# Kernel optimization log

Measured on AMD Instinct MI355X. Metric: run time of the kernel, lower is better.

Reference implementation:

```python
import jax, jax.numpy as jnp
import numpy as np

B, NPG, NFEAT, NHID, NCLASS = 32, 256, 128, 64, 6
N = B * NPG
E_PER = NPG * 16
C = 1.0
SQC = 1.0  # sqrt(c)
MIN_NORM = 1e-15
PROJ_EPS = 4e-3
LAMB = 1.0


def _norm(x):
    return jnp.clip(jnp.linalg.norm(x, axis=-1, keepdims=True), MIN_NORM)


def artanh(x):
    x = jnp.clip(x, -1.0 + 1e-7, 1.0 - 1e-7)
    return 0.5 * (jnp.log1p(x) - jnp.log1p(-x))


def proj(x):
    # clip points to stay inside the Poincare ball
    n = _norm(x)
    maxn = (1.0 - PROJ_EPS) / SQC
    return jnp.where(n > maxn, x / n * maxn, x)


def expmap0(u):
    un = _norm(u)
    return jnp.tanh(SQC * un) * u / (SQC * un)


def logmap0(p):
    pn = _norm(p)
    return artanh(SQC * pn) * p / (SQC * pn)


def mobius_matvec(W, x):
    xn = _norm(x)
    mx = x @ W.T
    mxn = _norm(mx)
    return jnp.tanh(mxn / xn * artanh(SQC * xn)) * mx / (mxn * SQC)


def mobius_add(x, y):
    x2 = jnp.sum(x * x, -1, keepdims=True)
    y2 = jnp.sum(y * y, -1, keepdims=True)
    xy = jnp.sum(x * y, -1, keepdims=True)
    num = (1.0 + 2.0 * C * xy + C * y2) * x + (1.0 - C * x2) * y
    den = 1.0 + 2.0 * C * xy + C * C * x2 * y2
    return num / jnp.clip(den, MIN_NORM)


def hgc_layer(xh, adj, W, b):
    # HypLinear (mobius matvec + hyperbolic bias)
    h = proj(mobius_matvec(W, xh))
    hb = proj(expmap0(b.reshape(1, -1)))
    h = proj(mobius_add(h, hb))
    # HypAgg: aggregate in tangent space at origin
    h = proj(expmap0(adj @ logmap0(h)))
    # HypAct: relu in tangent space
    return proj(expmap0(jax.nn.relu(logmap0(h))))


def hgpsl_pool(x, adj, att, nb, npg):
    deg = adj.sum(-1)
    dis = jnp.where(deg > 0, deg ** -0.5, 0.0)
    prop = dis[:, None] * (adj @ (dis[:, None] * x))
    score = jnp.abs(x - prop).sum(-1)  # [N]
    k = npg // 2
    vals, idx = jax.lax.top_k(score.reshape(nb, npg), k)  # per-graph top-k
    gidx = (idx + (jnp.arange(nb) * npg)[:, None]).reshape(-1)  # global ids
    xn = x[gidx] * jnp.tanh(vals).reshape(-1, 1)
    adj_ind = adj[gidx][:, gidx]
    # structure learning: single-head additive attention, masked per graph
    d = xn.shape[-1]
    e = jax.nn.leaky_relu((xn @ att[:d])[:, None] + (xn @ att[d:])[None, :], 0.2)
    gid = jnp.repeat(jnp.arange(nb), k)
    mask = gid[:, None] == gid[None, :]
    new_adj = jnp.where(mask, jax.nn.relu(e) + LAMB * adj_ind, 0.0)
    return xn, new_adj


def readout(x, nb, k):
    xr = x.reshape(nb, k, -1)
    return jnp.concatenate([xr.max(axis=1), xr.mean(axis=1)], axis=-1)


def to_hyp(t):
    return proj(expmap0(t))  # proj_tan0 is identity on the Poincare ball


def forward(x, edge_index, W1, b1, W2, b2, W3, b3, att1, att2,
            lw1, lb1, lw2, lb2, lw3, lb3):
    row, col = edge_index[0], edge_index[1]
    w = (x[row].sum(-1) + x[col].sum(-1)) * 0.5
    adj1 = jnp.zeros((N, N), x.dtype).at[row, col].set(w)

    t = logmap0(hgc_layer(to_hyp(x), adj1, W1, b1))
    t, adj2 = hgpsl_pool(t, adj1, att1, B, NPG)
    k1 = NPG // 2
    x1 = readout(t, B, k1)

    t = logmap0(hgc_layer(to_hyp(t), adj2, W2, b2))
    t, adj3 = hgpsl_pool(t, adj2, att2, B, k1)
    k2 = k1 // 2
    x2 = readout(t, B, k2)

    t = logmap0(hgc_layer(to_hyp(t), adj3, W3, b3))
    x3 = readout(t, B, k2)

    r = jax.nn.relu(x1) + jax.nn.relu(x2) + jax.nn.relu(x3)
    r = jax.nn.relu(r @ lw1.T + lb1)
    r = jax.nn.relu(r @ lw2.T + lb2)
    return jax.nn.log_softmax(r @ lw3.T + lb3, axis=-1)


def setup_inputs() -> dict:
    key = jax.random.key(0)
    ks = jax.random.split(key, 16)
    s = 0.1
    x = jax.random.normal(ks[0], (N, NFEAT), jnp.float32)
    off = jnp.repeat(jnp.arange(B, dtype=jnp.int32) * NPG, E_PER)
    row = jax.random.randint(ks[1], (B * E_PER,), 0, NPG, jnp.int32) + off
    col = jax.random.randint(ks[2], (B * E_PER,), 0, NPG, jnp.int32) + off
    edge_index = jnp.stack([row, col])
    return {
        "x": x,
        "edge_index": edge_index,
        "W1": jax.random.normal(ks[3], (NHID, NFEAT), jnp.float32) * s,
        "b1": jax.random.normal(ks[4], (NHID,), jnp.float32) * s,
        "W2": jax.random.normal(ks[5], (NHID, NHID), jnp.float32) * s,
        "b2": jax.random.normal(ks[6], (NHID,), jnp.float32) * s,
        "W3": jax.random.normal(ks[7], (NHID, NHID), jnp.float32) * s,
        "b3": jax.random.normal(ks[8], (NHID,), jnp.float32) * s,
        "att1": jax.random.normal(ks[9], (2 * NHID,), jnp.float32) * s,
        "att2": jax.random.normal(ks[10], (2 * NHID,), jnp.float32) * s,
        "lw1": jax.random.normal(ks[11], (NHID, 2 * NHID), jnp.float32) * s,
        "lb1": jnp.zeros((NHID,), jnp.float32),
        "lw2": jax.random.normal(ks[12], (NHID // 2, NHID), jnp.float32) * s,
        "lb2": jnp.zeros((NHID // 2,), jnp.float32),
        "lw3": jax.random.normal(ks[13], (NCLASS, NHID // 2), jnp.float32) * s,
        "lb3": jnp.zeros((NCLASS,), jnp.float32),
    }


def reference(x, edge_index, W1, b1, W2, b2, W3, b3, att1, att2,
              lw1, lb1, lw2, lb2, lw3, lb3):
    return forward(x, edge_index, W1, b1, W2, b2, W3, b3, att1, att2,
                   lw1, lb1, lw2, lb2, lw3, lb3)
```

## Files before the change

### kernel.cpp

```cpp
#include <hip/hip_runtime.h>
#include <math.h>

#define MAXN 0.996f

__device__ __forceinline__ float wredsum(float v) {
#pragma unroll
  for (int o = 32; o > 0; o >>= 1) v += __shfl_xor(v, o);
  return v;
}

__device__ __forceinline__ float artanh_f(float x) {
  x = fminf(fmaxf(x, -1.0f + 1e-7f), 1.0f - 1e-7f);
  return 0.5f * (log1pf(x) - log1pf(-x));
}

__device__ __forceinline__ float cload(const float* p) {
  return __hip_atomic_load(p, __ATOMIC_RELAXED, __HIP_MEMORY_SCOPE_AGENT);
}
__device__ __forceinline__ int cloadi(const int* p) {
  return __hip_atomic_load(p, __ATOMIC_RELAXED, __HIP_MEMORY_SCOPE_AGENT);
}
__device__ __forceinline__ void cstore(float* p, float v) {
  __hip_atomic_store(p, v, __ATOMIC_RELAXED, __HIP_MEMORY_SCOPE_AGENT);
}
__device__ __forceinline__ void cstorei(int* p, int v) {
  __hip_atomic_store(p, v, __ATOMIC_RELAXED, __HIP_MEMORY_SCOPE_AGENT);
}
__device__ __forceinline__ void cstore64(float* p, float lo, float hi) {
  unsigned long long u =
      ((unsigned long long)__float_as_uint(hi) << 32) | __float_as_uint(lo);
  __hip_atomic_store((unsigned long long*)p, u, __ATOMIC_RELAXED,
                     __HIP_MEMORY_SCOPE_AGENT);
}
__device__ __forceinline__ void pairStore(float* base, int j, float v) {
  float o = __shfl_xor(v, 1);
  if ((j & 1) == 0) cstore64(base + j, v, o);
}
template <int N>
__device__ __forceinline__ void stage64(float* dst, const float* src, int tid) {
  const unsigned long long* s = (const unsigned long long*)src;
  unsigned long long* d = (unsigned long long*)dst;
  unsigned long long v[N];
#pragma unroll
  for (int k = 0; k < N; ++k)
    v[k] = __hip_atomic_load(s + tid + k * 1024, __ATOMIC_RELAXED,
                             __HIP_MEMORY_SCOPE_AGENT);
#pragma unroll
  for (int k = 0; k < N; ++k) d[tid + k * 1024] = v[k];
}

__device__ __forceinline__ float chainB(float acc) {
  float n0 = sqrtf(wredsum(acc * acc));
  float u0 = fmaxf(n0, 1e-15f);
  float e1 = tanhf(u0) / u0;
  float c1 = fmaxf(e1 * n0, 1e-15f);
  float v = acc * e1;
  if (c1 > MAXN) { v *= MAXN / c1; c1 = MAXN; }
  v *= artanh_f(c1) / c1;
  v = fmaxf(v, 0.f);
  float n2 = sqrtf(wredsum(v * v));
  float u2 = fmaxf(n2, 1e-15f);
  float e2 = tanhf(u2) / u2;
  float c2 = fmaxf(e2 * n2, 1e-15f);
  v *= e2;
  if (c2 > MAXN) { v *= MAXN / c2; c2 = MAXN; }
  v *= artanh_f(c2) / c2;
  return v;
}

__device__ __forceinline__ void hbCalc(int j, const float* __restrict__ b,
                                       float& hbj, float& y2) {
  float bj = b[j];
  float nb = sqrtf(wredsum(bj * bj));
  float ub = fmaxf(nb, 1e-15f);
  float eb = tanhf(ub) / ub;
  float cb = fmaxf(eb * nb, 1e-15f);
  hbj = bj * eb * ((cb > MAXN) ? MAXN / cb : 1.0f);
  y2 = wredsum(hbj * hbj);
}

template <int IND>
__device__ __forceinline__ void doArow(int j, const float* xs, const float* wT,
                                       float hbj, float y2,
                                       float* __restrict__ uout) {
  float a2 = xs[j] * xs[j];
  if (IND == 128) { float x1v = xs[64 + j]; a2 += x1v * x1v; }
  float nx = sqrtf(wredsum(a2));
  float un = fmaxf(nx, 1e-15f);
  float s1 = tanhf(un) / un;
  float nv = s1 * nx;
  float nn = fmaxf(nv, 1e-15f);
  float s2 = (nn > MAXN) ? MAXN / nn : 1.0f;
  float alpha = s1 * s2;
  float xn = fmaxf(fminf(nn, MAXN), 1e-15f);

  float y = 0.f;
  for (int t = 0; t < IND; ++t) y = fmaf(xs[t], wT[t * 65 + j], y);
  float mxj = alpha * y;
  float mxn = fmaxf(sqrtf(wredsum(mxj * mxj)), 1e-15f);
  float hj = (tanhf(mxn / xn * artanh_f(xn)) / mxn) * mxj;

  float hn = fmaxf(sqrtf(wredsum(hj * hj)), 1e-15f);
  if (hn > MAXN) hj *= MAXN / hn;

  float x2 = wredsum(hj * hj);
  float xy = wredsum(hj * hbj);
  float num = (1.f + 2.f * xy + y2) * hj + (1.f - x2) * hbj;
  float den = fmaxf(1.f + 2.f * xy + x2 * y2, 1e-15f);
  float aj = num / den;

  float an = fmaxf(sqrtf(wredsum(aj * aj)), 1e-15f);
  float pn = an;
  if (an > MAXN) { aj *= MAXN / an; pn = MAXN; }
  pairStore(uout, j, (artanh_f(pn) / pn) * aj);
}

template <int NP, int TR, bool WANTDIS>
__device__ __forceinline__ void doBgrpL(int j, int r0, int r0l,
                                        const float* adjS, const float* uS,
                                        float* __restrict__ tg,
                                        float* __restrict__ disg) {
  float acc[TR], dsum[TR];
#pragma unroll
  for (int r = 0; r < TR; ++r) { acc[r] = 0.f; dsum[r] = 0.f; }
  for (int c0 = 0; c0 < NP; c0 += 4) {
    float uv0 = uS[(c0 + 0) * 64 + j];
    float uv1 = uS[(c0 + 1) * 64 + j];
    float uv2 = uS[(c0 + 2) * 64 + j];
    float uv3 = uS[(c0 + 3) * 64 + j];
#pragma unroll
    for (int r = 0; r < TR; ++r) {
      const float4 a4 = *(const float4*)(adjS + (r0l + r) * NP + c0);
      acc[r] = fmaf(a4.x, uv0, acc[r]);
      acc[r] = fmaf(a4.y, uv1, acc[r]);
      acc[r] = fmaf(a4.z, uv2, acc[r]);
      acc[r] = fmaf(a4.w, uv3, acc[r]);
      if (WANTDIS) {
        dsum[r] += a4.x; dsum[r] += a4.y; dsum[r] += a4.z; dsum[r] += a4.w;
      }
    }
  }
#pragma unroll
  for (int r = 0; r < TR; ++r) {
    float v = chainB(acc[r]);
    pairStore(tg + (size_t)(r0 + r) * 64, j, v);
    if (WANTDIS && j == 0)
      cstore(disg + r0 + r, (dsum[r] > 0.f) ? (1.0f / sqrtf(dsum[r])) : 0.f);
  }
}

template <int NP, int TR>
__device__ __forceinline__ void doCgrpL(int j, int r0, int r0l,
                                        const float* adjS, const float* tS,
                                        const float* disS,
                                        float* __restrict__ scoreg) {
  float acc[TR];
#pragma unroll
  for (int r = 0; r < TR; ++r) acc[r] = 0.f;
  for (int c0 = 0; c0 < NP; c0 += 4) {
    float uv0 = disS[c0 + 0] * tS[(c0 + 0) * 64 + j];
    float uv1 = disS[c0 + 1] * tS[(c0 + 1) * 64 + j];
    float uv2 = disS[c0 + 2] * tS[(c0 + 2) * 64 + j];
    float uv3 = disS[c0 + 3] * tS[(c0 + 3) * 64 + j];
#pragma unroll
    for (int r = 0; r < TR; ++r) {
      const float4 a4 = *(const float4*)(adjS + (r0l + r) * NP + c0);
      acc[r] = fmaf(a4.x, uv0, acc[r]);
      acc[r] = fmaf(a4.y, uv1, acc[r]);
      acc[r] = fmaf(a4.z, uv2, acc[r]);
      acc[r] = fmaf(a4.w, uv3, acc[r]);
    }
  }
#pragma unroll
  for (int r = 0; r < TR; ++r) {
    float d = fabsf(tS[(r0 + r) * 64 + j] - disS[r0 + r] * acc[r]);
    d = wredsum(d);
    if (j == 0) cstore(scoreg + r0 + r, d);
  }
}

template <int NP>
__device__ __forceinline__ void doDEa(int j, int i, const float* scS,
                                      const float* tS,
                                      const float* __restrict__ att,
                                      float* __restrict__ xng,
                                      float* __restrict__ s1g,
                                      float* __restrict__ s2g,
                                      int* __restrict__ selg) {
  constexpr int K = NP / 2;
  float si = scS[i];
  float cnt = 0.f;
#pragma unroll
  for (int kk = 0; kk < NP / 64; ++kk) {
    int c = j + kk * 64;
    float v = scS[c];
    cnt += ((v > si) || (v == si && c < i)) ? 1.f : 0.f;
  }
  int rank = (int)wredsum(cnt);
  if (rank < K) {
    float tv = tanhf(si);
    float v = tS[i * 64 + j] * tv;
    pairStore(xng + (size_t)rank * 64, j, v);
    float a = wredsum(v * att[j]);
    float b2 = wredsum(v * att[64 + j]);
    if (j == 0) {
      cstore(s1g + rank, a);
      cstore(s2g + rank, b2);
      cstorei(selg + rank, i);
    }
  }
}

template <int K>
__device__ __forceinline__ void doReadout(int j, const float* __restrict__ xng,
                                          float* __restrict__ xrg) {
  float mx = -1e30f, sm = 0.f;
#pragma unroll
  for (int r = 0; r < K; ++r) {
    float v = cload(xng + (size_t)r * 64 + j);
    mx = fmaxf(mx, v);
    sm += v;
  }
  cstore(xrg + j, mx);
  cstore(xrg + 64 + j, sm * (1.0f / K));
}

__device__ __forceinline__ void cluster_bar(int* bar, int target, int tid) {
  __syncthreads();
  if (tid == 0) {
    __hip_atomic_fetch_add(bar, 1, __ATOMIC_RELAXED, __HIP_MEMORY_SCOPE_AGENT);
    while (__hip_atomic_load(bar, __ATOMIC_RELAXED, __HIP_MEMORY_SCOPE_AGENT) <
           target * 8)
      __builtin_amdgcn_s_sleep(2);
  }
  __syncthreads();
}

struct KP {
  const float* x; const int* ei; int nE;
  const float *W1, *b1, *W2, *b2, *W3, *b3, *att1, *att2;
  const float *lw1, *lb1, *lw2, *lb2, *lw3, *lb3;
  float *adj2, *adj3, *ubuf, *t1, *t2, *t3, *dis, *score;
  float *xn1, *xn2, *s1b, *s2b, *x1, *x2;
  int *sel, *bar;
  float* out;
};

__global__ void __launch_bounds__(1024, 4) k_fwd(KP P) {
  const int tid = threadIdx.x;
  const int wib = tid >> 6;
  const int j = tid & 63;
  const int g = blockIdx.x >> 3;
  const int lb = blockIdx.x & 7;
  const int wc = lb * 16 + wib;

  __shared__ float wT[128 * 65];
  __shared__ float xsAll[16 * 128];
  __shared__ float stage[16384];
  __shared__ float adjS[8192];
  __shared__ float scS[256];
  __shared__ float s1S[128];
  __shared__ float s2S[128];
  __shared__ int selS[128];
  float* xs = xsAll + wib * 128;

  int* bar = P.bar + g * 64;
  float* adj2g = P.adj2 + (size_t)g * 16384;
  float* adj3g = P.adj3 + (size_t)g * 4096;
  const float* xg = P.x + (size_t)g * 32768;
  float* ubufg = P.ubuf + (size_t)g * 16384;
  float* t1g = P.t1 + (size_t)g * 16384;
  float* t2g = P.t2 + (size_t)g * 8192;
  float* t3g = P.t3 + (size_t)g * 4096;
  float* disg = P.dis + g * 256;
  float* scoreg = P.score + g * 256;
  float* xn1g = P.xn1 + (size_t)g * 8192;
  float* xn2g = P.xn2 + (size_t)g * 4096;
  float* s1g = P.s1b + g * 128;
  float* s2g = P.s2b + g * 128;
  int* selg = P.sel + g * 128;
  float* x1g = P.x1 + g * 128;
  float* x2g = P.x2 + g * 128;

  {
    for (int idx = tid; idx < 8192; idx += 1024)
      wT[(idx & 127) * 65 + (idx >> 7)] = P.W1[idx];
    for (int row = wib * 16; row < wib * 16 + 16; ++row) {
      float a = xg[(size_t)row * 128 + j] + xg[(size_t)row * 128 + 64 + j];
      a = wredsum(a);
      if (j == 0) scS[row] = a;
    }
    for (int k = tid; k < 8192; k += 1024) adjS[k] = 0.f;
    __syncthreads();
    const int epg = P.nE >> 5;
    for (int e = g * epg + tid; e < (g + 1) * epg; e += 1024) {
      int r = P.ei[e] & 255;
      if ((r >> 5) == lb) {
        int c = P.ei[P.nE + e] & 255;
        adjS[(r & 31) * 256 + c] = 0.5f * (scS[r] + scS[c]);
      }
    }
    float hbj, y2;
    hbCalc(j, P.b1, hbj, y2);
    for (int row = wc; row < 256; row += 128) {
      xs[j] = xg[(size_t)row * 128 + j];
      xs[64 + j] = xg[(size_t)row * 128 + 64 + j];
      doArow<128>(j, xs, wT, hbj, y2, ubufg + (size_t)row * 64);
    }
  }
  cluster_bar(bar, 1, tid);

  {
    stage64<8>(stage, ubufg, tid);
    __syncthreads();
    doBgrpL<256, 2, true>(j, wc * 2, wib * 2, adjS, stage, t1g, disg);
    for (int idx = tid; idx < 4096; idx += 1024)
      wT[(idx & 63) * 65 + (idx >> 6)] = P.W2[idx];
  }
  cluster_bar(bar, 2, tid);

  {
    if (tid < 256) scS[tid] = cload(disg + tid);
    stage64<8>(stage, t1g, tid);
    __syncthreads();
    doCgrpL<256, 2>(j, wc * 2, wib * 2, adjS, stage, scS, scoreg);
  }
  cluster_bar(bar, 3, tid);

  {
    if (tid < 256) scS[tid] = cload(scoreg + tid);
    __syncthreads();
    for (int row = wc; row < 256; row += 128)
      doDEa<256>(j, row, scS, stage, P.att1, xn1g, s1g, s2g, selg);
  }
  cluster_bar(bar, 4, tid);

  {
    if (tid < 128) {
      s1S[tid] = cload(s1g + tid);
      s2S[tid] = cload(s2g + tid);
      selS[tid] = cloadi(selg + tid);
    }
    __syncthreads();
    for (int idx2 = tid; idx2 < 8192; idx2 += 1024) {
      int ii = idx2 >> 6, jp = idx2 & 63;
      int sii = selS[ii];
      if ((sii >> 5) == lb) {
        int jj0 = jp * 2;
        const float* arow = adjS + (sii & 31) * 256;
        float v0 = fmaxf(s1S[ii] + s2S[jj0], 0.f) + arow[selS[jj0]];
        float v1 = fmaxf(s1S[ii] + s2S[jj0 + 1], 0.f) + arow[selS[jj0 + 1]];
        cstore64(adj2g + ii * 128 + jj0, v0, v1);
      }
    }
    if (wc == 0) doReadout<128>(j, xn1g, x1g);
    float hbj, y2;
    hbCalc(j, P.b2, hbj, y2);
    {
      int row = wc;
      xs[j] = cload(xn1g + (size_t)row * 64 + j);
      doArow<64>(j, xs, wT, hbj, y2, ubufg + (size_t)row * 64);
    }
  }
  cluster_bar(bar, 5, tid);

  {
    stage64<1>(adjS, adj2g + lb * 2048, tid);
    stage64<4>(stage, ubufg, tid);
    __syncthreads();
    doBgrpL<128, 1, true>(j, wc, wib, adjS, stage, t2g, disg);
    for (int idx = tid; idx < 4096; idx += 1024)
      wT[(idx & 63) * 65 + (idx >> 6)] = P.W3[idx];
  }
  cluster_bar(bar, 6, tid);

  {
    if (tid < 128) scS[tid] = cload(disg + tid);
    stage64<4>(stage, t2g, tid);
    __syncthreads();
    doCgrpL<128, 1>(j, wc, wib, adjS, stage, scS, scoreg);
  }
  cluster_bar(bar, 7, tid);

  {
    if (tid < 128) scS[tid] = cload(scoreg + tid);
    __syncthreads();
    doDEa<128>(j, wc, scS, stage, P.att2, xn2g, s1g, s2g, selg);
  }
  cluster_bar(bar, 8, tid);

  {
    if (tid < 64) {
      s1S[tid] = cload(s1g + tid);
      s2S[tid] = cload(s2g + tid);
      selS[tid] = cloadi(selg + tid);
    }
    __syncthreads();
    for (int idx2 = tid; idx2 < 2048; idx2 += 1024) {
      int ii = idx2 >> 5, jp = idx2 & 31;
      int sii = selS[ii];
      if ((sii >> 4) == lb) {
        int jj0 = jp * 2;
        const float* arow = adjS + (sii & 15) * 128;
        float v0 = fmaxf(s1S[ii] + s2S[jj0], 0.f) + arow[selS[jj0]];
        float v1 = fmaxf(s1S[ii] + s2S[jj0 + 1], 0.f) + arow[selS[jj0 + 1]];
        cstore64(adj3g + ii * 64 + jj0, v0, v1);
      }
    }
    if (wc == 0) doReadout<64>(j, xn2g, x2g);
    float hbj, y2;
    hbCalc(j, P.b3, hbj, y2);
    if (wc < 64) {
      int row = wc;
      xs[j] = cload(xn2g + (size_t)row * 64 + j);
      doArow<64>(j, xs, wT, hbj, y2, ubufg + (size_t)row * 64);
    }
  }
  cluster_bar(bar, 9, tid);

  if (lb < 4) {
    if (tid < 512) {
      unsigned long long v = __hip_atomic_load(
          (const unsigned long long*)(adj3g + lb * 1024) + tid,
          __ATOMIC_RELAXED, __HIP_MEMORY_SCOPE_AGENT);
      ((unsigned long long*)adjS)[tid] = v;
    }
    stage64<2>(stage, ubufg, tid);
    __syncthreads();
    doBgrpL<64, 1, false>(j, wc, wib, adjS, stage, t3g, nullptr);
  }
  cluster_bar(bar, 10, tid);

  if (wc == 0) {
    float mx = -1e30f, sm = 0.f;
#pragma unroll
    for (int r = 0; r < 64; ++r) {
      float v = cload(t3g + (size_t)r * 64 + j);
      mx = fmaxf(mx, v);
      sm += v;
    }
    float* S = xsAll;
    S[j] = fmaxf(cload(x1g + j), 0.f) + fmaxf(cload(x2g + j), 0.f) +
           fmaxf(mx, 0.f);
    S[64 + j] = fmaxf(cload(x1g + 64 + j), 0.f) +
                fmaxf(cload(x2g + 64 + j), 0.f) +
                fmaxf(sm * (1.0f / 64.0f), 0.f);
    float acc = P.lb1[j];
    for (int t = 0; t < 128; ++t) acc += S[t] * P.lw1[(size_t)j * 128 + t];
    S[128 + j] = fmaxf(acc, 0.f);
    if (j < 32) {
      float a = P.lb2[j];
      for (int t = 0; t < 64; ++t) a += S[128 + t] * P.lw2[(size_t)j * 64 + t];
      S[192 + j] = fmaxf(a, 0.f);
    }
    if (j < 6) {
      float a = P.lb3[j];
      for (int t = 0; t < 32; ++t) a += S[192 + t] * P.lw3[(size_t)j * 32 + t];
      S[224 + j] = a;
    }
    if (j < 6) {
      float m = S[224];
      for (int c = 1; c < 6; ++c) m = fmaxf(m, S[224 + c]);
      float se = 0.f;
      for (int c = 0; c < 6; ++c) se += expf(S[224 + c] - m);
      P.out[(size_t)g * 6 + j] = S[224 + j] - m - logf(se);
    }
  }
}

extern "C" void kernel_launch(void* const* d_in, const int* in_sizes, int n_in,
                              void* d_out, int out_size, void* d_ws,
                              size_t ws_size, hipStream_t stream) {
  KP hp;
  hp.x = (const float*)d_in[0];
  hp.ei = (const int*)d_in[1];
  hp.nE = in_sizes[1] / 2;
  hp.W1 = (const float*)d_in[2];
  hp.b1 = (const float*)d_in[3];
  hp.W2 = (const float*)d_in[4];
  hp.b2 = (const float*)d_in[5];
  hp.W3 = (const float*)d_in[6];
  hp.b3 = (const float*)d_in[7];
  hp.att1 = (const float*)d_in[8];
  hp.att2 = (const float*)d_in[9];
  hp.lw1 = (const float*)d_in[10];
  hp.lb1 = (const float*)d_in[11];
  hp.lw2 = (const float*)d_in[12];
  hp.lb2 = (const float*)d_in[13];
  hp.lw3 = (const float*)d_in[14];
  hp.lb3 = (const float*)d_in[15];
  hp.out = (float*)d_out;

  float* p = (float*)d_ws;
  hp.adj2 = p;  p += (size_t)32 * 16384;
  hp.adj3 = p;  p += (size_t)32 * 4096;
  hp.ubuf = p;  p += (size_t)32 * 16384;
  hp.t1 = p;    p += (size_t)32 * 16384;
  hp.t2 = p;    p += (size_t)32 * 8192;
  hp.t3 = p;    p += (size_t)32 * 4096;
  hp.dis = p;   p += 32 * 256;
  hp.score = p; p += 32 * 256;
  hp.xn1 = p;   p += (size_t)32 * 8192;
  hp.xn2 = p;   p += (size_t)32 * 4096;
  hp.s1b = p;   p += 32 * 128;
  hp.s2b = p;   p += 32 * 128;
  hp.x1 = p;    p += 32 * 128;
  hp.x2 = p;    p += 32 * 128;
  hp.sel = (int*)p; p += 32 * 128;
  hp.bar = (int*)p; p += 32 * 64;

  hipMemsetAsync(hp.bar, 0, 32 * 64 * sizeof(int), stream);
  k_fwd<<<256, 1024, 0, stream>>>(hp);
}
```

Baseline: 213.0 us.

## Distribute row-sum work, widen stores to dwordx4, keep readouts in LDS

Each cooperating block now computes row sums only for its own 32 rows. The sums go to a global buffer that is read back after the first barrier, replacing the old scheme where every block redundantly read the whole graph's features. Pair stores via 64-bit atomics become 128-bit global_store_dwordx4 with sc0/sc1 cache bits, built from three lane shuffles. The pooled readouts now stay in shared memory, since the same block performs the final MLP, which drops global round-trips. The costs are extra shuffles and inline asm that relies on sc0/sc1 semantics for cross-block visibility.

```diff
diff --git a/kernel.cpp b/kernel.cpp
--- a/kernel.cpp
+++ b/kernel.cpp
@@ -2,6 +2,8 @@
 #include <math.h>
 
 #define MAXN 0.996f
+
+typedef float f32x4 __attribute__((ext_vector_type(4)));
 
 __device__ __forceinline__ float wredsum(float v) {
 #pragma unroll
@@ -26,15 +28,18 @@
 __device__ __forceinline__ void cstorei(int* p, int v) {
   __hip_atomic_store(p, v, __ATOMIC_RELAXED, __HIP_MEMORY_SCOPE_AGENT);
 }
-__device__ __forceinline__ void cstore64(float* p, float lo, float hi) {
-  unsigned long long u =
-      ((unsigned long long)__float_as_uint(hi) << 32) | __float_as_uint(lo);
-  __hip_atomic_store((unsigned long long*)p, u, __ATOMIC_RELAXED,
-                     __HIP_MEMORY_SCOPE_AGENT);
-}
-__device__ __forceinline__ void pairStore(float* base, int j, float v) {
-  float o = __shfl_xor(v, 1);
-  if ((j & 1) == 0) cstore64(base + j, v, o);
+__device__ __forceinline__ void cstore128(float* p, float a, float b, float c,
+                                          float d) {
+  f32x4 v;
+  v.x = a; v.y = b; v.z = c; v.w = d;
+  asm volatile("global_store_dwordx4 %0, %1, off sc0 sc1" ::"v"(p), "v"(v)
+               : "memory");
+}
+__device__ __forceinline__ void quadStore(float* base, int j, float v) {
+  float v1 = __shfl_xor(v, 1);
+  float v2 = __shfl_xor(v, 2);
+  float v3 = __shfl_xor(v, 3);
+  if ((j & 3) == 0) cstore128(base + j, v, v1, v2, v3);
 }
 template <int N>
 __device__ __forceinline__ void stage64(float* dst, const float* src, int tid) {
@@ -112,7 +117,7 @@
   float an = fmaxf(sqrtf(wredsum(aj * aj)), 1e-15f);
   float pn = an;
   if (an > MAXN) { aj *= MAXN / an; pn = MAXN; }
-  pairStore(uout, j, (artanh_f(pn) / pn) * aj);
+  quadStore(uout, j, (artanh_f(pn) / pn) * aj);
 }
 
 template <int NP, int TR, bool WANTDIS>
@@ -143,7 +148,7 @@
 #pragma unroll
   for (int r = 0; r < TR; ++r) {
     float v = chainB(acc[r]);
-    pairStore(tg + (size_t)(r0 + r) * 64, j, v);
+    quadStore(tg + (size_t)(r0 + r) * 64, j, v);
     if (WANTDIS && j == 0)
       cstore(disg + r0 + r, (dsum[r] > 0.f) ? (1.0f / sqrtf(dsum[r])) : 0.f);
   }
@@ -200,7 +205,7 @@
   if (rank < K) {
     float tv = tanhf(si);
     float v = tS[i * 64 + j] * tv;
-    pairStore(xng + (size_t)rank * 64, j, v);
+    quadStore(xng + (size_t)rank * 64, j, v);
     float a = wredsum(v * att[j]);
     float b2 = wredsum(v * att[64 + j]);
     if (j == 0) {
@@ -212,8 +217,8 @@
 }
 
 template <int K>
-__device__ __forceinline__ void doReadout(int j, const float* __restrict__ xng,
-                                          float* __restrict__ xrg) {
+__device__ __forceinline__ void doReadoutL(int j, const float* __restrict__ xng,
+                                           float* xrl) {
   float mx = -1e30f, sm = 0.f;
 #pragma unroll
   for (int r = 0; r < K; ++r) {
@@ -221,8 +226,8 @@
     mx = fmaxf(mx, v);
     sm += v;
   }
-  cstore(xrg + j, mx);
-  cstore(xrg + 64 + j, sm * (1.0f / K));
+  xrl[j] = mx;
+  xrl[64 + j] = sm * (1.0f / K);
 }
 
 __device__ __forceinline__ void cluster_bar(int* bar, int target, int tid) {
@@ -240,8 +245,8 @@
   const float* x; const int* ei; int nE;
   const float *W1, *b1, *W2, *b2, *W3, *b3, *att1, *att2;
   const float *lw1, *lb1, *lw2, *lb2, *lw3, *lb3;
-  float *adj2, *adj3, *ubuf, *t1, *t2, *t3, *dis, *score;
-  float *xn1, *xn2, *s1b, *s2b, *x1, *x2;
+  float *adj2, *adj3, *ubuf, *t1, *t2, *t3, *srow, *dis, *score;
+  float *xn1, *xn2, *s1b, *s2b;
   int *sel, *bar;
   float* out;
 };
@@ -262,12 +267,14 @@
   __shared__ float s1S[128];
   __shared__ float s2S[128];
   __shared__ int selS[128];
+  __shared__ float x12S[256];
   float* xs = xsAll + wib * 128;
 
   int* bar = P.bar + g * 64;
   float* adj2g = P.adj2 + (size_t)g * 16384;
   float* adj3g = P.adj3 + (size_t)g * 4096;
   const float* xg = P.x + (size_t)g * 32768;
+  float* srowg = P.srow + g * 256;
   float* ubufg = P.ubuf + (size_t)g * 16384;
   float* t1g = P.t1 + (size_t)g * 16384;
   float* t2g = P.t2 + (size_t)g * 8192;
@@ -279,18 +286,28 @@
   float* s1g = P.s1b + g * 128;
   float* s2g = P.s2b + g * 128;
   int* selg = P.sel + g * 128;
-  float* x1g = P.x1 + g * 128;
-  float* x2g = P.x2 + g * 128;
 
   {
     for (int idx = tid; idx < 8192; idx += 1024)
       wT[(idx & 127) * 65 + (idx >> 7)] = P.W1[idx];
-    for (int row = wib * 16; row < wib * 16 + 16; ++row) {
-      float a = xg[(size_t)row * 128 + j] + xg[(size_t)row * 128 + 64 + j];
+    for (int k = tid; k < 8192; k += 1024) adjS[k] = 0.f;
+    float hbj, y2;
+    hbCalc(j, P.b1, hbj, y2);
+    for (int rr = 0; rr < 2; ++rr) {
+      const int row = lb * 32 + wib * 2 + rr;
+      xs[j] = xg[(size_t)row * 128 + j];
+      xs[64 + j] = xg[(size_t)row * 128 + 64 + j];
+      float a = xs[j] + xs[64 + j];
       a = wredsum(a);
-      if (j == 0) scS[row] = a;
-    }
-    for (int k = tid; k < 8192; k += 1024) adjS[k] = 0.f;
+      if (j == 0) cstore(srowg + row, a);
+      doArow<128>(j, xs, wT, hbj, y2, ubufg + (size_t)row * 64);
+    }
+  }
+  cluster_bar(bar, 1, tid);
+
+  {
+    if (tid < 256) scS[tid] = cload(srowg + tid);
+    stage64<8>(stage, ubufg, tid);
     __syncthreads();
     const int epg = P.nE >> 5;
     for (int e = g * epg + tid; e < (g + 1) * epg; e += 1024) {
@@ -300,20 +317,9 @@
         adjS[(r & 31) * 256 + c] = 0.5f * (scS[r] + scS[c]);
       }
     }
-    float hbj, y2;
-    hbCalc(j, P.b1, hbj, y2);
-    for (int row = wc; row < 256; row += 128) {
-      xs[j] = xg[(size_t)row * 128 + j];
-      xs[64 + j] = xg[(size_t)row * 128 + 64 + j];
-      doArow<128>(j, xs, wT, hbj, y2, ubufg + (size_t)row * 64);
-    }
-  }
-  cluster_bar(bar, 1, tid);
-
-  {
-    stage64<8>(stage, ubufg, tid);
-    __syncthreads();
-    doBgrpL<256, 2, true>(j, wc * 2, wib * 2, adjS, stage, t1g, disg);
+    __syncthreads();
+    doBgrpL<256, 2, true>(j, lb * 32 + wib * 2, wib * 2, adjS, stage, t1g,
+                          disg);
     for (int idx = tid; idx < 4096; idx += 1024)
       wT[(idx & 63) * 65 + (idx >> 6)] = P.W2[idx];
   }
@@ -323,7 +329,7 @@
     if (tid < 256) scS[tid] = cload(disg + tid);
     stage64<8>(stage, t1g, tid);
     __syncthreads();
-    doCgrpL<256, 2>(j, wc * 2, wib * 2, adjS, stage, scS, scoreg);
+    doCgrpL<256, 2>(j, lb * 32 + wib * 2, wib * 2, adjS, stage, scS, scoreg);
   }
   cluster_bar(bar, 3, tid);
 
@@ -342,18 +348,20 @@
       selS[tid] = cloadi(selg + tid);
     }
     __syncthreads();
-    for (int idx2 = tid; idx2 < 8192; idx2 += 1024) {
-      int ii = idx2 >> 6, jp = idx2 & 63;
+    for (int q = tid; q < 4096; q += 1024) {
+      int ii = q >> 5, jj0 = (q & 31) * 4;
       int sii = selS[ii];
       if ((sii >> 5) == lb) {
-        int jj0 = jp * 2;
         const float* arow = adjS + (sii & 31) * 256;
-        float v0 = fmaxf(s1S[ii] + s2S[jj0], 0.f) + arow[selS[jj0]];
-        float v1 = fmaxf(s1S[ii] + s2S[jj0 + 1], 0.f) + arow[selS[jj0 + 1]];
-        cstore64(adj2g + ii * 128 + jj0, v0, v1);
+        float s1v = s1S[ii];
+        float v0 = fmaxf(s1v + s2S[jj0 + 0], 0.f) + arow[selS[jj0 + 0]];
+        float v1 = fmaxf(s1v + s2S[jj0 + 1], 0.f) + arow[selS[jj0 + 1]];
+        float v2 = fmaxf(s1v + s2S[jj0 + 2], 0.f) + arow[selS[jj0 + 2]];
+        float v3 = fmaxf(s1v + s2S[jj0 + 3], 0.f) + arow[selS[jj0 + 3]];
+        cstore128(adj2g + ii * 128 + jj0, v0, v1, v2, v3);
       }
     }
-    if (wc == 0) doReadout<128>(j, xn1g, x1g);
+    if (wc == 0) doReadoutL<128>(j, xn1g, x12S);
     float hbj, y2;
     hbCalc(j, P.b2, hbj, y2);
     {
@@ -396,18 +404,20 @@
       selS[tid] = cloadi(selg + tid);
     }
     __syncthreads();
-    for (int idx2 = tid; idx2 < 2048; idx2 += 1024) {
-      int ii = idx2 >> 5, jp = idx2 & 31;
+    {
+      int ii = tid >> 4, jj0 = (tid & 15) * 4;
       int sii = selS[ii];
       if ((sii >> 4) == lb) {
-        int jj0 = jp * 2;
         const float* arow = adjS + (sii & 15) * 128;
-        float v0 = fmaxf(s1S[ii] + s2S[jj0], 0.f) + arow[selS[jj0]];
-        float v1 = fmaxf(s1S[ii] + s2S[jj0 + 1], 0.f) + arow[selS[jj0 + 1]];
-        cstore64(adj3g + ii * 64 + jj0, v0, v1);
+        float s1v = s1S[ii];
+        float v0 = fmaxf(s1v + s2S[jj0 + 0], 0.f) + arow[selS[jj0 + 0]];
+        float v1 = fmaxf(s1v + s2S[jj0 + 1], 0.f) + arow[selS[jj0 + 1]];
+        float v2 = fmaxf(s1v + s2S[jj0 + 2], 0.f) + arow[selS[jj0 + 2]];
+        float v3 = fmaxf(s1v + s2S[jj0 + 3], 0.f) + arow[selS[jj0 + 3]];
+        cstore128(adj3g + ii * 64 + jj0, v0, v1, v2, v3);
       }
     }
-    if (wc == 0) doReadout<64>(j, xn2g, x2g);
+    if (wc == 0) doReadoutL<64>(j, xn2g, x12S + 128);
     float hbj, y2;
     hbCalc(j, P.b3, hbj, y2);
     if (wc < 64) {
@@ -440,10 +450,8 @@
       sm += v;
     }
     float* S = xsAll;
-    S[j] = fmaxf(cload(x1g + j), 0.f) + fmaxf(cload(x2g + j), 0.f) +
-           fmaxf(mx, 0.f);
-    S[64 + j] = fmaxf(cload(x1g + 64 + j), 0.f) +
-                fmaxf(cload(x2g + 64 + j), 0.f) +
+    S[j] = fmaxf(x12S[j], 0.f) + fmaxf(x12S[128 + j], 0.f) + fmaxf(mx, 0.f);
+    S[64 + j] = fmaxf(x12S[64 + j], 0.f) + fmaxf(x12S[192 + j], 0.f) +
                 fmaxf(sm * (1.0f / 64.0f), 0.f);
     float acc = P.lb1[j];
     for (int t = 0; t < 128; ++t) acc += S[t] * P.lw1[(size_t)j * 128 + t];
@@ -498,14 +506,13 @@
   hp.t1 = p;    p += (size_t)32 * 16384;
   hp.t2 = p;    p += (size_t)32 * 8192;
   hp.t3 = p;    p += (size_t)32 * 4096;
+  hp.srow = p;  p += 32 * 256;
   hp.dis = p;   p += 32 * 256;
   hp.score = p; p += 32 * 256;
   hp.xn1 = p;   p += (size_t)32 * 8192;
   hp.xn2 = p;   p += (size_t)32 * 4096;
   hp.s1b = p;   p += 32 * 128;
   hp.s2b = p;   p += 32 * 128;
-  hp.x1 = p;    p += 32 * 128;
-  hp.x2 = p;    p += 32 * 128;
   hp.sel = (int*)p; p += 32 * 128;
   hp.bar = (int*)p; p += 32 * 64;
 
```

Result: faster. 208.0 us, median of 3 (-2.3%).
